# Performance work log

Hardware: AMD Instinct MI355X
Metric: run time of the kernel (lower is better)

## Reference

```python
import jax, jax.numpy as jnp
import numpy as np

B, T, H = 256, 512, 1024


def _xavier(key, shape, gain=1.0):
    fan_in, fan_out = shape[1], shape[0]
    limit = gain * np.sqrt(6.0 / (fan_in + fan_out))
    return jax.random.uniform(key, shape, jnp.float32, -limit, limit)


def setup_inputs() -> dict:
    key = jax.random.key(0)
    ks = jax.random.split(key, 8)
    x = jax.random.normal(ks[0], (B, T, H), jnp.float32)
    ht = jax.random.normal(ks[1], (B, H), jnp.float32)
    # nn.Linear weights are [out, in]; xavier gain 1.0 for Wz/Uz/Wh/Uh, 1.667 for Wr/Ur
    Wz = _xavier(ks[2], (H, H), 1.0)
    Uz = _xavier(ks[3], (H, H), 1.0)
    Wr = _xavier(ks[4], (H, H), 1.667)
    Ur = _xavier(ks[5], (H, H), 1.667)
    Wh = _xavier(ks[6], (H, H), 1.0)
    Uh = _xavier(ks[7], (H, H), 1.0)
    return {"x": x, "ht": ht, "Wz": Wz, "Uz": Uz, "Wr": Wr, "Ur": Ur, "Wh": Wh, "Uh": Uh}


def reference(x, ht, Wz, Uz, Wr, Ur, Wh, Uh):
    # Precompute the input-side projections for all timesteps in two big GEMMs
    # (same math as per-step Wz(x_i)/Wh(x_i), just batched). Note: the original
    # forward computes a reset gate r but never uses it, so it is omitted —
    # identical output.
    xz = jnp.einsum('bti,oi->tbo', x, Wz)  # [T, B, H]
    xh = jnp.einsum('bti,oi->tbo', x, Wh)  # [T, B, H]

    def step(h, xs):
        xz_t, xh_t = xs
        z = jax.nn.sigmoid(xz_t + h @ Uz.T)
        h_ = jnp.tanh(xh_t + h @ Uh.T)
        h = z * h + (1.0 - z) * h_
        return h, None

    h_final, _ = jax.lax.scan(step, ht, (xz, xh))
    return (h_final, h_final)
```

## Files before the change

kernel.cpp:

```cpp
#include <hip/hip_runtime.h>

typedef unsigned short u16;
typedef unsigned int u32;
typedef __bf16 bf16x8 __attribute__((ext_vector_type(8)));
typedef float f32x4 __attribute__((ext_vector_type(4)));
typedef float f32x16 __attribute__((ext_vector_type(16)));
typedef u16 u16x4 __attribute__((ext_vector_type(4)));
typedef u16 u16x8 __attribute__((ext_vector_type(8)));

#define HDIM 1024
#define BATCH 256
#define TSTEPS 512
#define BT (BATCH * TSTEPS)
#define HB_ELEMS (BATCH * HDIM)

__device__ __forceinline__ u16 f2bf(float f) {
  union { float f; u32 u; } v; v.f = f;
  u32 r = v.u + 0x7FFFu + ((v.u >> 16) & 1u);
  return (u16)(r >> 16);
}
__device__ __forceinline__ float bf2f(u16 u) {
  union { u32 u; float f; } v; v.u = ((u32)u) << 16;
  return v.f;
}

__device__ __forceinline__ void gload_lds16(const void* g, void* l) {
  __builtin_amdgcn_global_load_lds(
      (const __attribute__((address_space(1))) unsigned int*)g,
      (__attribute__((address_space(3))) unsigned int*)l, 16, 0, 0);
}

__global__ __launch_bounds__(256) void pack_kernel(
    const float* __restrict__ Wz, const float* __restrict__ Uz,
    const float* __restrict__ Wh, const float* __restrict__ Uh,
    const float* __restrict__ ht,
    u16* __restrict__ Wcat, u16* __restrict__ Ucat,
    float* __restrict__ hf0, u16* __restrict__ hb0,
    u32* __restrict__ cnt)
{
  if (blockIdx.x == 0 && threadIdx.x < 16) cnt[threadIdx.x] = 0;
  const long M = 1L << 20;
  long e = ((long)blockIdx.x * 256 + threadIdx.x) * 4;
  const float* src;
  u16* dst;
  if (e < M)            { src = Wz + e;        dst = Wcat + e; }
  else if (e < 2 * M)   { src = Wh + (e - M);  dst = Wcat + e; }
  else if (e < 3 * M)   { src = Uz + (e - 2*M); dst = Ucat + (e - 2*M); }
  else if (e < 4 * M)   { src = Uh + (e - 3*M); dst = Ucat + (e - 2*M); }
  else {
    long j = e - 4 * M;
    float4 v = *(const float4*)(ht + j);
    *(float4*)(hf0 + j) = v;
    u16x4 o = { f2bf(v.x), f2bf(v.y), f2bf(v.z), f2bf(v.w) };
    *(u16x4*)(hb0 + j) = o;
    return;
  }
  float4 v = *(const float4*)src;
  u16x4 o = { f2bf(v.x), f2bf(v.y), f2bf(v.z), f2bf(v.w) };
  *(u16x4*)dst = o;
}

__global__ __launch_bounds__(256) void gemm_xw(
    const float* __restrict__ x, const u16* __restrict__ Wcat,
    u16* __restrict__ xzh)
{
  __shared__ u16 As[128 * 64];
  __shared__ u16 Bs[128 * 64];

  const int NWG = (BT / 128) * (2048 / 128);
  int bid = blockIdx.x;
  int swz = (bid & 7) * (NWG / 8) + (bid >> 3);
  int tm = swz >> 4;
  int tn = swz & 15;
  long m0 = (long)tm * 128;
  int n0 = tn * 128;

  int tid = threadIdx.x;
  int w = tid >> 6, l = tid & 63;
  int wr = (w >> 1) * 64;
  int wc = (w & 1) * 64;

  f32x4 acc[4][4] = {};

  const int arow = tid >> 3;
  const int acol = (tid & 7) * 8;
  const int brow = l >> 3;
  const int bcol = (l & 7) * 8;

  for (int kc = 0; kc < 16; ++kc) {
    int k0 = kc * 64;
#pragma unroll
    for (int j = 0; j < 4; ++j) {
      int r = (w * 4 + j) * 8 + brow;
      gload_lds16(Wcat + (((long)(n0 + r)) << 10) + k0 + bcol,
                  &Bs[(w * 4 + j) * 512]);
    }
    float4 av[4][2];
#pragma unroll
    for (int s = 0; s < 4; ++s) {
      const float* src = x + ((m0 + arow + s * 32) << 10) + k0 + acol;
      av[s][0] = *(const float4*)src;
      av[s][1] = *(const float4*)(src + 4);
    }
#pragma unroll
    for (int s = 0; s < 4; ++s) {
      u16x8 o = { f2bf(av[s][0].x), f2bf(av[s][0].y), f2bf(av[s][0].z), f2bf(av[s][0].w),
                  f2bf(av[s][1].x), f2bf(av[s][1].y), f2bf(av[s][1].z), f2bf(av[s][1].w) };
      *(u16x8*)(As + tid * 8 + s * 2048) = o;
    }
    __syncthreads();
#pragma unroll
    for (int kk = 0; kk < 2; ++kk) {
      int kb = kk * 32 + (l >> 4) * 8;
      int rr = l & 15;
      bf16x8 af[4], bfr[4];
#pragma unroll
      for (int i = 0; i < 4; ++i)
        af[i] = *(const bf16x8*)(As + (wr + i * 16 + rr) * 64 + kb);
#pragma unroll
      for (int j = 0; j < 4; ++j)
        bfr[j] = *(const bf16x8*)(Bs + (wc + j * 16 + rr) * 64 + kb);
#pragma unroll
      for (int i = 0; i < 4; ++i)
#pragma unroll
        for (int j = 0; j < 4; ++j)
          acc[i][j] = __builtin_amdgcn_mfma_f32_16x16x32_bf16(af[i], bfr[j], acc[i][j], 0, 0, 0);
    }
    __syncthreads();
  }

  int rq = (l >> 4) * 4;
  int rc = l & 15;
#pragma unroll
  for (int i = 0; i < 4; ++i) {
#pragma unroll
    for (int r = 0; r < 4; ++r) {
      long m = m0 + wr + i * 16 + rq + r;
      int b = (int)(m >> 9);
      int t = (int)(m & 511);
      u16* dst = xzh + (((long)t * 256 + b) << 11);
#pragma unroll
      for (int j = 0; j < 4; ++j)
        dst[n0 + wc + j * 16 + rc] = f2bf(acc[i][j][r]);
    }
  }
}

__global__ __launch_bounds__(256) void gru_scan(
    const u16* __restrict__ Ucat, const u16* __restrict__ xzh,
    u16* __restrict__ hb, float* __restrict__ hf,
    u32* __restrict__ cnt, float* __restrict__ outp)
{
  __shared__ u16 BL[2][32][1024];
  __shared__ float red[3][2][1024];

  int bid = blockIdx.x;
  int g = bid & 7;
  int j = bid >> 3;
  int b0 = g * 32;
  int o0 = j * 32;
  int tid = threadIdx.x;
  int w = tid >> 6;
  int l = tid & 63;
  int hi = l >> 5;
  int col = l & 31;
  const int colx = (l & 7) << 4;

#pragma unroll 1
  for (int gate = 0; gate < 2; ++gate) {
    const u16* src = Ucat + (((long)gate << 20) + ((long)o0 << 10));
    char* dstbase = (char*)&BL[gate][0][0];
#pragma unroll
    for (int i = 0; i < 16; ++i) {
      int c = i * 256 + tid;
      int row = c >> 7;
      int inner = (c & 127) << 4;
      u16x8 v = *(const u16x8*)(src + row * 1024 + (inner >> 1));
      *(u16x8*)(dstbase + row * 2048 + (inner ^ ((row & 7) << 4))) = v;
    }
  }
  __syncthreads();

  const char* bz_base = (const char*)&BL[0][0][0] + col * 2048;
  const char* bh_base = (const char*)&BL[1][0][0] + col * 2048;
  const int kbase = (w << 9) + (hi << 4);

#pragma unroll 1
  for (int t = 0; t < TSTEPS; ++t) {
    int cur = t & 1;
    const u16* hbC = hb + cur * HB_ELEMS;
    const float* hfC = hf + cur * HB_ELEMS;
    u16* hbN = hb + (cur ^ 1) * HB_ELEMS;
    float* hfN = hf + (cur ^ 1) * HB_ELEMS;
    const u16* xt = xzh + (long)t * (BATCH * 2048);

    if (t > 0) {
      if (tid == 0) {
        u32 target = (u32)(32 * t);
        while (__hip_atomic_load(cnt + g, __ATOMIC_ACQUIRE,
                                 __HIP_MEMORY_SCOPE_AGENT) < target) {
          __builtin_amdgcn_s_sleep(1);
        }
      }
      __syncthreads();
    }

    bf16x8 a[16];
    const u16* hrow = hbC + ((long)(b0 + col) << 10) + (w << 8) + (hi << 3);
#pragma unroll
    for (int ks = 0; ks < 16; ++ks)
      a[ks] = *(const bf16x8*)(hrow + ks * 16);

    u16 xzv[16], xhv[16];
    float holdv[16];
    if (w == 0) {
#pragma unroll
      for (int r = 0; r < 16; ++r) {
        int row = (r & 3) + ((r >> 2) << 3) + (hi << 2);
        long bq = b0 + row;
        xzv[r] = xt[(bq << 11) + o0 + col];
        xhv[r] = xt[(bq << 11) + 1024 + o0 + col];
        holdv[r] = hfC[(bq << 10) + o0 + col];
      }
    }

    f32x16 accZ = {};
    f32x16 accH = {};
#pragma unroll
    for (int ks = 0; ks < 16; ++ks) {
      int koff = (kbase + ks * 32) ^ colx;
      bf16x8 bz = *(const bf16x8*)(bz_base + koff);
      bf16x8 bh = *(const bf16x8*)(bh_base + koff);
      accZ = __builtin_amdgcn_mfma_f32_32x32x16_bf16(a[ks], bz, accZ, 0, 0, 0);
      accH = __builtin_amdgcn_mfma_f32_32x32x16_bf16(a[ks], bh, accH, 0, 0, 0);
    }

    if (w != 0) {
      float* rb = &red[w - 1][0][0];
#pragma unroll
      for (int q = 0; q < 4; ++q) {
        f32x4 vz = { accZ[q*4+0], accZ[q*4+1], accZ[q*4+2], accZ[q*4+3] };
        f32x4 vh = { accH[q*4+0], accH[q*4+1], accH[q*4+2], accH[q*4+3] };
        *(f32x4*)(rb + q * 256 + l * 4) = vz;
        *(f32x4*)(rb + 1024 + q * 256 + l * 4) = vh;
      }
    }
    __syncthreads();

    if (w == 0) {
#pragma unroll
      for (int i = 0; i < 3; ++i) {
        const float* rb = &red[i][0][0];
#pragma unroll
        for (int q = 0; q < 4; ++q) {
          f32x4 vz = *(const f32x4*)(rb + q * 256 + l * 4);
          f32x4 vh = *(const f32x4*)(rb + 1024 + q * 256 + l * 4);
          accZ[q*4+0] += vz[0]; accZ[q*4+1] += vz[1];
          accZ[q*4+2] += vz[2]; accZ[q*4+3] += vz[3];
          accH[q*4+0] += vh[0]; accH[q*4+1] += vh[1];
          accH[q*4+2] += vh[2]; accH[q*4+3] += vh[3];
        }
      }
      bool last = (t == TSTEPS - 1);
#pragma unroll
      for (int r = 0; r < 16; ++r) {
        int row = (r & 3) + ((r >> 2) << 3) + (hi << 2);
        long bq = b0 + row;
        float zp = accZ[r] + bf2f(xzv[r]);
        float hp = accH[r] + bf2f(xhv[r]);
        float z = 1.f / (1.f + __expf(-zp));
        float th = tanhf(hp);
        float hnew = z * holdv[r] + (1.f - z) * th;
        if (last) {
          outp[(bq << 10) + o0 + col] = hnew;
          outp[(long)HB_ELEMS + (bq << 10) + o0 + col] = hnew;
        } else {
          hfN[(bq << 10) + o0 + col] = hnew;
          hbN[(bq << 10) + o0 + col] = f2bf(hnew);
        }
      }
      if (!last && tid == 0) {
        __hip_atomic_fetch_add(cnt + g, 1u, __ATOMIC_RELEASE,
                               __HIP_MEMORY_SCOPE_AGENT);
      }
    }
  }
}

extern "C" void kernel_launch(void* const* d_in, const int* in_sizes, int n_in,
                              void* d_out, int out_size, void* d_ws, size_t ws_size,
                              hipStream_t stream)
{
  const float* x  = (const float*)d_in[0];
  const float* ht = (const float*)d_in[1];
  const float* Wz = (const float*)d_in[2];
  const float* Uz = (const float*)d_in[3];
  const float* Wh = (const float*)d_in[6];
  const float* Uh = (const float*)d_in[7];

  char* ws = (char*)d_ws;
  u16*   xzh  = (u16*)ws;
  u16*   Wcat = (u16*)(ws + 536870912L);
  u16*   Ucat = (u16*)(ws + 541065216L);
  float* hf   = (float*)(ws + 545259520L);
  u16*   hb   = (u16*)(ws + 547356672L);
  u32*   cnt  = (u32*)(ws + 548405248L);

  pack_kernel<<<4352, 256, 0, stream>>>(Wz, Uz, Wh, Uh, ht, Wcat, Ucat, hf, hb, cnt);
  gemm_xw<<<16384, 256, 0, stream>>>(x, Wcat, xzh);
  gru_scan<<<256, 256, 0, stream>>>(Ucat, xzh, hb, hf, cnt, (float*)d_out);
}
```

Before: 8.799 ms.

## Distribute GRU epilogue across all waves, keep fp32 state in registers

The reduction of partial MFMA accumulators now spreads across all four waves: each wave owns one quarter of the rows and sums the other waves' partials, where previously wave 0 did all of it. The fp32 hidden state stays in registers for the whole scan, so the global fp32 h buffer and its per-step reload go away. The xz/xh loads are issued before the inter-block barrier wait so they overlap it. The h exchange uses relaxed atomic loads and stores with explicit fences, and the per-group counters are padded onto separate cache lines. The cost is an extra __syncthreads per step before signalling, and the correctness of the relaxed-atomic plus fence ordering is subtle.

```diff
diff --git a/kernel.cpp b/kernel.cpp
--- a/kernel.cpp
+++ b/kernel.cpp
@@ -2,6 +2,7 @@
 
 typedef unsigned short u16;
 typedef unsigned int u32;
+typedef unsigned long long u64;
 typedef __bf16 bf16x8 __attribute__((ext_vector_type(8)));
 typedef float f32x4 __attribute__((ext_vector_type(4)));
 typedef float f32x16 __attribute__((ext_vector_type(16)));
@@ -22,6 +23,16 @@
 __device__ __forceinline__ float bf2f(u16 u) {
   union { u32 u; float f; } v; v.u = ((u32)u) << 16;
   return v.f;
+}
+
+__device__ __forceinline__ bf16x8 ald16(const u16* p) {
+  union { u64 q[2]; bf16x8 v; } u;
+  u.q[0] = __hip_atomic_load((const u64*)p, __ATOMIC_RELAXED, __HIP_MEMORY_SCOPE_AGENT);
+  u.q[1] = __hip_atomic_load((const u64*)p + 1, __ATOMIC_RELAXED, __HIP_MEMORY_SCOPE_AGENT);
+  return u.v;
+}
+__device__ __forceinline__ void ast2(u16* p, u16 v) {
+  __hip_atomic_store(p, v, __ATOMIC_RELAXED, __HIP_MEMORY_SCOPE_AGENT);
 }
 
 __device__ __forceinline__ void gload_lds16(const void* g, void* l) {
@@ -38,7 +49,7 @@
     float* __restrict__ hf0, u16* __restrict__ hb0,
     u32* __restrict__ cnt)
 {
-  if (blockIdx.x == 0 && threadIdx.x < 16) cnt[threadIdx.x] = 0;
+  if (blockIdx.x == 0) { cnt[threadIdx.x] = 0; cnt[threadIdx.x + 256] = 0; }
   const long M = 1L << 20;
   long e = ((long)blockIdx.x * 256 + threadIdx.x) * 4;
   const float* src;
@@ -148,11 +159,11 @@
 
 __global__ __launch_bounds__(256) void gru_scan(
     const u16* __restrict__ Ucat, const u16* __restrict__ xzh,
-    u16* __restrict__ hb, float* __restrict__ hf,
+    const float* __restrict__ hf0, u16* __restrict__ hb,
     u32* __restrict__ cnt, float* __restrict__ outp)
 {
   __shared__ u16 BL[2][32][1024];
-  __shared__ float red[3][2][1024];
+  __shared__ float red[4][3][2][256];
 
   int bid = blockIdx.x;
   int g = bid & 7;
@@ -165,6 +176,7 @@
   int hi = l >> 5;
   int col = l & 31;
   const int colx = (l & 7) << 4;
+  u32* cg = cnt + (g << 6);
 
 #pragma unroll 1
   for (int gate = 0; gate < 2; ++gate) {
@@ -179,6 +191,13 @@
       *(u16x8*)(dstbase + row * 2048 + (inner ^ ((row & 7) << 4))) = v;
     }
   }
+
+  float hold[4];
+#pragma unroll
+  for (int rr = 0; rr < 4; ++rr) {
+    int row = 8 * w + rr + 4 * hi;
+    hold[rr] = hf0[(((long)(b0 + row)) << 10) + o0 + col];
+  }
   __syncthreads();
 
   const char* bz_base = (const char*)&BL[0][0][0] + col * 2048;
@@ -189,18 +208,25 @@
   for (int t = 0; t < TSTEPS; ++t) {
     int cur = t & 1;
     const u16* hbC = hb + cur * HB_ELEMS;
-    const float* hfC = hf + cur * HB_ELEMS;
     u16* hbN = hb + (cur ^ 1) * HB_ELEMS;
-    float* hfN = hf + (cur ^ 1) * HB_ELEMS;
     const u16* xt = xzh + (long)t * (BATCH * 2048);
+
+    u16 xzv[4], xhv[4];
+#pragma unroll
+    for (int rr = 0; rr < 4; ++rr) {
+      long bq = b0 + 8 * w + rr + 4 * hi;
+      xzv[rr] = xt[(bq << 11) + o0 + col];
+      xhv[rr] = xt[(bq << 11) + 1024 + o0 + col];
+    }
 
     if (t > 0) {
       if (tid == 0) {
         u32 target = (u32)(32 * t);
-        while (__hip_atomic_load(cnt + g, __ATOMIC_ACQUIRE,
+        while (__hip_atomic_load(cg, __ATOMIC_RELAXED,
                                  __HIP_MEMORY_SCOPE_AGENT) < target) {
           __builtin_amdgcn_s_sleep(1);
         }
+        __threadfence();
       }
       __syncthreads();
     }
@@ -209,20 +235,7 @@
     const u16* hrow = hbC + ((long)(b0 + col) << 10) + (w << 8) + (hi << 3);
 #pragma unroll
     for (int ks = 0; ks < 16; ++ks)
-      a[ks] = *(const bf16x8*)(hrow + ks * 16);
-
-    u16 xzv[16], xhv[16];
-    float holdv[16];
-    if (w == 0) {
-#pragma unroll
-      for (int r = 0; r < 16; ++r) {
-        int row = (r & 3) + ((r >> 2) << 3) + (hi << 2);
-        long bq = b0 + row;
-        xzv[r] = xt[(bq << 11) + o0 + col];
-        xhv[r] = xt[(bq << 11) + 1024 + o0 + col];
-        holdv[r] = hfC[(bq << 10) + o0 + col];
-      }
-    }
+      a[ks] = ald16(hrow + ks * 16);
 
     f32x16 accZ = {};
     f32x16 accH = {};
@@ -235,52 +248,62 @@
       accH = __builtin_amdgcn_mfma_f32_32x32x16_bf16(a[ks], bh, accH, 0, 0, 0);
     }
 
-    if (w != 0) {
-      float* rb = &red[w - 1][0][0];
-#pragma unroll
-      for (int q = 0; q < 4; ++q) {
-        f32x4 vz = { accZ[q*4+0], accZ[q*4+1], accZ[q*4+2], accZ[q*4+3] };
-        f32x4 vh = { accH[q*4+0], accH[q*4+1], accH[q*4+2], accH[q*4+3] };
-        *(f32x4*)(rb + q * 256 + l * 4) = vz;
-        *(f32x4*)(rb + 1024 + q * 256 + l * 4) = vh;
+#pragma unroll
+    for (int d = 0; d < 4; ++d) {
+      if (d == w) continue;
+      int s = (w > d) ? (w - 1) : w;
+      f32x4 vz = { accZ[4*d+0], accZ[4*d+1], accZ[4*d+2], accZ[4*d+3] };
+      f32x4 vh = { accH[4*d+0], accH[4*d+1], accH[4*d+2], accH[4*d+3] };
+      *(f32x4*)&red[d][s][0][l * 4] = vz;
+      *(f32x4*)&red[d][s][1][l * 4] = vh;
+    }
+    __syncthreads();
+
+    f32x4 az, ah;
+    if (w == 0) {
+      az = f32x4{accZ[0], accZ[1], accZ[2], accZ[3]};
+      ah = f32x4{accH[0], accH[1], accH[2], accH[3]};
+    } else if (w == 1) {
+      az = f32x4{accZ[4], accZ[5], accZ[6], accZ[7]};
+      ah = f32x4{accH[4], accH[5], accH[6], accH[7]};
+    } else if (w == 2) {
+      az = f32x4{accZ[8], accZ[9], accZ[10], accZ[11]};
+      ah = f32x4{accH[8], accH[9], accH[10], accH[11]};
+    } else {
+      az = f32x4{accZ[12], accZ[13], accZ[14], accZ[15]};
+      ah = f32x4{accH[12], accH[13], accH[14], accH[15]};
+    }
+#pragma unroll
+    for (int s = 0; s < 3; ++s) {
+      f32x4 vz = *(const f32x4*)&red[w][s][0][l * 4];
+      f32x4 vh = *(const f32x4*)&red[w][s][1][l * 4];
+      az += vz;
+      ah += vh;
+    }
+
+    bool last = (t == TSTEPS - 1);
+#pragma unroll
+    for (int rr = 0; rr < 4; ++rr) {
+      long bq = b0 + 8 * w + rr + 4 * hi;
+      float zp = az[rr] + bf2f(xzv[rr]);
+      float hp = ah[rr] + bf2f(xhv[rr]);
+      float z = 1.f / (1.f + __expf(-zp));
+      float th = tanhf(hp);
+      float hnew = z * hold[rr] + (1.f - z) * th;
+      hold[rr] = hnew;
+      if (last) {
+        outp[(bq << 10) + o0 + col] = hnew;
+        outp[(long)HB_ELEMS + (bq << 10) + o0 + col] = hnew;
+      } else {
+        ast2(&hbN[(bq << 10) + o0 + col], f2bf(hnew));
       }
     }
-    __syncthreads();
-
-    if (w == 0) {
-#pragma unroll
-      for (int i = 0; i < 3; ++i) {
-        const float* rb = &red[i][0][0];
-#pragma unroll
-        for (int q = 0; q < 4; ++q) {
-          f32x4 vz = *(const f32x4*)(rb + q * 256 + l * 4);
-          f32x4 vh = *(const f32x4*)(rb + 1024 + q * 256 + l * 4);
-          accZ[q*4+0] += vz[0]; accZ[q*4+1] += vz[1];
-          accZ[q*4+2] += vz[2]; accZ[q*4+3] += vz[3];
-          accH[q*4+0] += vh[0]; accH[q*4+1] += vh[1];
-          accH[q*4+2] += vh[2]; accH[q*4+3] += vh[3];
-        }
-      }
-      bool last = (t == TSTEPS - 1);
-#pragma unroll
-      for (int r = 0; r < 16; ++r) {
-        int row = (r & 3) + ((r >> 2) << 3) + (hi << 2);
-        long bq = b0 + row;
-        float zp = accZ[r] + bf2f(xzv[r]);
-        float hp = accH[r] + bf2f(xhv[r]);
-        float z = 1.f / (1.f + __expf(-zp));
-        float th = tanhf(hp);
-        float hnew = z * holdv[r] + (1.f - z) * th;
-        if (last) {
-          outp[(bq << 10) + o0 + col] = hnew;
-          outp[(long)HB_ELEMS + (bq << 10) + o0 + col] = hnew;
-        } else {
-          hfN[(bq << 10) + o0 + col] = hnew;
-          hbN[(bq << 10) + o0 + col] = f2bf(hnew);
-        }
-      }
-      if (!last && tid == 0) {
-        __hip_atomic_fetch_add(cnt + g, 1u, __ATOMIC_RELEASE,
+
+    if (!last) {
+      __syncthreads();
+      if (tid == 0) {
+        __threadfence();
+        __hip_atomic_fetch_add(cg, 1u, __ATOMIC_RELAXED,
                                __HIP_MEMORY_SCOPE_AGENT);
       }
     }
@@ -302,11 +325,11 @@
   u16*   xzh  = (u16*)ws;
   u16*   Wcat = (u16*)(ws + 536870912L);
   u16*   Ucat = (u16*)(ws + 541065216L);
-  float* hf   = (float*)(ws + 545259520L);
-  u16*   hb   = (u16*)(ws + 547356672L);
-  u32*   cnt  = (u32*)(ws + 548405248L);
-
-  pack_kernel<<<4352, 256, 0, stream>>>(Wz, Uz, Wh, Uh, ht, Wcat, Ucat, hf, hb, cnt);
+  float* hf0  = (float*)(ws + 545259520L);
+  u16*   hb   = (u16*)(ws + 546308096L);
+  u32*   cnt  = (u32*)(ws + 547356672L);
+
+  pack_kernel<<<4352, 256, 0, stream>>>(Wz, Uz, Wh, Uh, ht, Wcat, Ucat, hf0, hb, cnt);
   gemm_xw<<<16384, 256, 0, stream>>>(x, Wcat, xzh);
-  gru_scan<<<256, 256, 0, stream>>>(Ucat, xzh, hb, hf, cnt, (float*)d_out);
-}
+  gru_scan<<<256, 256, 0, stream>>>(Ucat, xzh, hf0, hb, cnt, (float*)d_out);
+}
```

Result: slower. 11.32 ms (+28.7%).
